# Kernel tuning notes

Measured on AMD Instinct MI355X. Metric: run time of the kernel, lower is better.

## Reference

```python
import jax, jax.numpy as jnp
import numpy as np

jax.config.update("jax_enable_x64", True)  # faithful int64 LIF state, as in the torch module

NUM_INPUTS = 700
NUM_HIDDEN = 4096
NUM_OUTPUT = 20
N_STEPS = 1000
ALPHA_SHIFT = 4   # synaptic-current decay shift
BETA_SHIFT = 3    # membrane decay shift
THRESHOLD = 1
BW1 = 64
BW2 = 64


def _sat(x, bw):
    # Quantize.saturate + to_int: clamp to signed bw-bit range, cast to int64.
    lo = -(2 ** (bw - 1))
    hi = 2 ** (bw - 1) - 1
    if jnp.issubdtype(x.dtype, jnp.floating):
        # values here are far below 2**63, so the float clip/cast is exact
        return jnp.clip(x, float(lo), float(hi)).astype(jnp.int64)
    return jnp.clip(x, lo, hi)


def _decay(v, shift):
    # LIF.exp_decay: v - (v >> shift) with arithmetic right shift on int64
    return v - (v >> shift)


def setup_inputs() -> dict:
    key = jax.random.key(0)
    k1, k2, k3, k4 = jax.random.split(key, 4)
    input_spikes = jax.random.randint(k1, (N_STEPS, NUM_INPUTS), 0, 2, dtype=jnp.int64)
    w1 = jax.random.randint(k2, (NUM_HIDDEN, NUM_INPUTS), -8, 8, dtype=jnp.int64)
    v1 = jax.random.randint(k3, (NUM_HIDDEN, NUM_HIDDEN), -8, 8, dtype=jnp.int64)
    w2 = jax.random.randint(k4, (NUM_OUTPUT, NUM_HIDDEN), -8, 8, dtype=jnp.int64)
    return {"input_spikes": input_spikes, "w1": w1, "v1": v1, "w2": w2}


def reference(input_spikes, w1, v1, w2):
    w1f = w1.astype(jnp.float32)
    v1f = v1.astype(jnp.float32)
    w2f = w2.astype(jnp.float32)
    # feed-forward input currents for all timesteps at once: [T, H]
    in_all = _sat(jnp.einsum("hi,ti->th", w1f, input_spikes.astype(jnp.float32)), BW1)

    H = w1.shape[0]
    O = w2.shape[0]
    z = lambda n: jnp.zeros((n,), dtype=jnp.int64)
    # state: hidden spikes, hidden mem, hidden syn, readout mem, readout syn
    init = (z(H), z(H), z(H), z(O), z(O))

    def step(state, in_cur):
        h_out, h_mem, h_syn, r_mem, r_syn = state
        # recurrent feedback current from PREVIOUS step's hidden spikes
        fb = _sat(jnp.einsum("hk,k->h", v1f, h_out.astype(jnp.float32)), BW1)
        syn_curr = _sat(in_cur + fb, BW1)
        # hidden LIF: reset (by previous spike) -> threshold -> decay/integrate
        h_mem = jnp.where(h_out == 1, 0, h_mem)
        new_out = (h_mem - THRESHOLD > 0).astype(jnp.int64)
        new_mem = _decay(h_mem, BETA_SHIFT) + h_syn
        new_syn = _decay(h_syn, ALPHA_SHIFT) + syn_curr
        # readout LIF (no reset); records updated membrane
        ro_cur = _sat(jnp.einsum("oh,h->o", w2f, new_out.astype(jnp.float32)), BW2)
        new_rmem = _decay(r_mem, BETA_SHIFT) + r_syn
        new_rsyn = _decay(r_syn, ALPHA_SHIFT) + ro_cur
        return (new_out, new_mem, new_syn, new_rmem, new_rsyn), new_rmem

    _, rec = jax.lax.scan(step, init, in_all)  # rec: [T, O]
    return rec.T  # torch.stack(ro_mem_rec, dim=1) -> [num_output, n_steps]
```

## Files before the change

kernel.cpp:

```cpp
#include <hip/hip_runtime.h>

#define T_STEPS 1000
#define N_IN    700
#define N_HID   4096
#define N_OUT   20
#define NBLK    64
#define HPB     64

typedef unsigned int u32x4 __attribute__((ext_vector_type(4)));

__device__ __forceinline__ u32x4 load_rec(const u32x4* p) {
    u32x4 r;
    asm volatile("global_load_dwordx4 %0, %1, off sc0 sc1\n\t"
                 "s_waitcnt vmcnt(0)"
                 : "=v"(r) : "v"(p) : "memory");
    return r;
}
__device__ __forceinline__ void store_rec(u32x4* p, u32x4 v) {
    asm volatile("global_store_dwordx4 %0, %1, off sc0 sc1"
                 :: "v"(p), "v"(v) : "memory");
}

__global__ __launch_bounds__(256) void k_transpose_i8(
    const int* __restrict__ in, signed char* __restrict__ out,
    int R, int C, int out_stride)
{
    __shared__ signed char tile[32][33];
    const int cx = blockIdx.x * 32;
    const int ry = blockIdx.y * 32;
    const int tx = threadIdx.x;
    const int ty = threadIdx.y;
#pragma unroll
    for (int r = 0; r < 4; ++r) {
        int row = ry + ty + r * 8;
        int col = cx + tx;
        if (row < R && col < C)
            tile[ty + r * 8][tx] = (signed char)in[(size_t)row * C + col];
    }
    __syncthreads();
#pragma unroll
    for (int r = 0; r < 4; ++r) {
        int c   = cx + ty + r * 8;
        int row = ry + tx;
        if (c < C && row < R)
            out[(size_t)c * out_stride + row] = tile[tx][ty + r * 8];
    }
}

__global__ __launch_bounds__(256) void k_prep_v1(
    const int* __restrict__ in, unsigned char* __restrict__ out)
{
    __shared__ unsigned char tile[32][33];
    const int kx = blockIdx.x * 32;
    const int hy = blockIdx.y * 32;
    const int tx = threadIdx.x;
    const int ty = threadIdx.y;
#pragma unroll
    for (int r = 0; r < 4; ++r) {
        int h = hy + ty + r * 8;
        tile[ty + r * 8][tx] = (unsigned char)(in[(size_t)h * N_HID + kx + tx] + 8);
    }
    __syncthreads();
    const size_t bofs = (size_t)(hy >> 6) * (N_HID * 64) + (hy & 32);
#pragma unroll
    for (int r = 0; r < 4; ++r) {
        int k = kx + ty + r * 8;
        out[bofs + ((size_t)k << 6) + tx] = tile[tx][ty + r * 8];
    }
}

__global__ __launch_bounds__(256) void k_inall(
    const signed char* __restrict__ w1t,
    const int* __restrict__ spk,
    short* __restrict__ in_all)
{
    __shared__ int s_spk[16][N_IN];
    const int t0 = blockIdx.y * 16;
    const int tcnt = min(16, T_STEPS - t0);
    const int tid = threadIdx.x;
    for (int b = 0; b < tcnt; ++b)
        for (int i = tid; i < N_IN; i += 256)
            s_spk[b][i] = spk[(size_t)(t0 + b) * N_IN + i];
    __syncthreads();
    const int h = blockIdx.x * 256 + tid;
    int acc[16];
#pragma unroll
    for (int b = 0; b < 16; ++b) acc[b] = 0;
    for (int i = 0; i < N_IN; ++i) {
        int w = (int)w1t[(size_t)i * N_HID + h];
#pragma unroll
        for (int b = 0; b < 16; ++b) acc[b] += w * s_spk[b][i];
    }
    for (int b = 0; b < tcnt; ++b)
        in_all[(size_t)(t0 + b) * N_HID + h] = (short)acc[b];
}

__global__ __launch_bounds__(256) void k_main(
    const short* __restrict__ in_all,
    const unsigned char* __restrict__ v1b,
    u32x4* __restrict__ pub)
{
    const int tid  = threadIdx.x;
    const int wave = tid >> 6;
    const int lane = tid & 63;
    const int hb   = blockIdx.x * HPB;

    __shared__ unsigned short s_list[N_HID];
    __shared__ unsigned int s_part[4][4][8];
    __shared__ int s_n;

    int mt = 0, syn = 0, cur_out = 0;
    unsigned long long omask = 0;

    const unsigned char* gbase = v1b + ((size_t)blockIdx.x << 18) + ((lane & 3) << 4);
    const int wg = (wave << 4) | (lane >> 2);

    for (int t = 0; t < T_STEPS; ++t) {
        int in_cur = 0;
        if (wave == 0) {
            if (lane == 0) {
                u32x4 v = { (unsigned)omask, (unsigned)(omask >> 32), 1u, 0u };
                store_rec(pub + (size_t)t * NBLK + blockIdx.x, v);
            }
            in_cur = (int)in_all[(size_t)t * N_HID + hb + lane];
            unsigned long long kmask = 0;
            if (t > 0) {
                const u32x4* rec = pub + (size_t)(t - 1) * NBLK + lane;
                u32x4 r = load_rec(rec);
                while (r.z == 0u) { __builtin_amdgcn_s_sleep(1); r = load_rec(rec); }
                kmask = ((unsigned long long)r.y << 32) | (unsigned long long)r.x;
            }
            int cnt = __popcll(kmask);
            int inc = cnt;
#pragma unroll
            for (int d = 1; d < 64; d <<= 1) {
                int v = __shfl_up(inc, d);
                if (lane >= d) inc += v;
            }
            int p = inc - cnt;
            unsigned long long m = kmask;
            while (m) {
                s_list[p++] = (unsigned short)((lane << 6) | __builtin_ctzll(m));
                m &= m - 1;
            }
            if (lane == 63) s_n = inc;
        }
        __syncthreads();
        const int n = s_n;

        unsigned int a0=0,a1=0,a2=0,a3=0,a4=0,a5=0,a6=0,a7=0;
#pragma unroll 8
        for (int j = wg; j < n; j += 64) {
            int k = s_list[j];
            u32x4 v = *(const u32x4*)(gbase + ((size_t)k << 6));
            const unsigned int M = 0x00FF00FFu;
            a0 += v.x & M;  a1 += (v.x >> 8) & M;
            a2 += v.y & M;  a3 += (v.y >> 8) & M;
            a4 += v.z & M;  a5 += (v.z >> 8) & M;
            a6 += v.w & M;  a7 += (v.w >> 8) & M;
        }
#pragma unroll
        for (int s = 4; s <= 32; s <<= 1) {
            a0 += __shfl_xor(a0, s); a1 += __shfl_xor(a1, s);
            a2 += __shfl_xor(a2, s); a3 += __shfl_xor(a3, s);
            a4 += __shfl_xor(a4, s); a5 += __shfl_xor(a5, s);
            a6 += __shfl_xor(a6, s); a7 += __shfl_xor(a7, s);
        }
        if (lane < 4) {
            unsigned int* sp = s_part[wave][lane];
            sp[0]=a0; sp[1]=a1; sp[2]=a2; sp[3]=a3;
            sp[4]=a4; sp[5]=a5; sp[6]=a6; sp[7]=a7;
        }
        __syncthreads();

        if (wave == 0) {
            const int li = lane >> 4, b = lane & 15;
            const int c = ((b >> 2) << 1) | (b & 1);
            const int half = (b >> 1) & 1;
            unsigned int s = s_part[0][li][c] + s_part[1][li][c]
                           + s_part[2][li][c] + s_part[3][li][c];
            int fb = (int)((s >> (half << 4)) & 0xFFFFu) - 8 * n;

            int new_mem = (mt - (mt >> 3)) + syn;
            syn = (syn - (syn >> 4)) + in_cur + fb;
            mt = cur_out ? 0 : new_mem;
            cur_out = (mt - 1 > 0) ? 1 : 0;
            omask = __ballot(cur_out);
        }
    }
}

__global__ __launch_bounds__(256) void k_rocur(
    const int* __restrict__ w2,
    const u32x4* __restrict__ pub,
    int* __restrict__ ro)
{
    const int t = blockIdx.x;
    const int tid = threadIdx.x;
    __shared__ unsigned short s_list[N_HID];
    __shared__ int s_red[32][8];
    __shared__ int s_n;
    if (tid < 64) {
        u32x4 rec = pub[(size_t)t * NBLK + tid];
        unsigned long long m = (unsigned long long)rec.x |
                               ((unsigned long long)rec.y << 32);
        int cnt = __popcll(m);
        int inc = cnt;
#pragma unroll
        for (int d = 1; d < 64; d <<= 1) {
            int v = __shfl_up(inc, d);
            if (tid >= d) inc += v;
        }
        int p = inc - cnt;
        while (m) {
            s_list[p++] = (unsigned short)((tid << 6) | __builtin_ctzll(m));
            m &= m - 1;
        }
        if (tid == 63) s_n = inc;
    }
    __syncthreads();
    const int n = s_n;
    const int o = tid >> 3;
    const int r = tid & 7;
    if (o < N_OUT) {
        int acc = 0;
        for (int j = r; j < n; j += 8) acc += w2[(size_t)o * N_HID + s_list[j]];
        s_red[o][r] = acc;
    }
    __syncthreads();
    if (tid < N_OUT) {
        int acc = 0;
#pragma unroll
        for (int q = 0; q < 8; ++q) acc += s_red[tid][q];
        ro[(size_t)t * N_OUT + tid] = acc;
    }
}

#define CH 250
__global__ __launch_bounds__(256) void k_scan(const int* __restrict__ ro,
                                              int* __restrict__ out)
{
    __shared__ int s_ro[CH * N_OUT];
    const int tid = threadIdx.x;
    int rm = 0, rs = 0;
    for (int c = 0; c < T_STEPS / CH; ++c) {
        __syncthreads();
        for (int i = tid; i < CH * N_OUT; i += 256)
            s_ro[i] = ro[c * CH * N_OUT + i];
        __syncthreads();
        if (tid < N_OUT) {
            for (int j = 0; j < CH; ++j) {
                rm = (rm - (rm >> 3)) + rs;
                rs = (rs - (rs >> 4)) + s_ro[j * N_OUT + tid];
                out[tid * T_STEPS + c * CH + j] = rm;
            }
        }
    }
}

extern "C" void kernel_launch(void* const* d_in, const int* in_sizes, int n_in,
                              void* d_out, int out_size, void* d_ws, size_t ws_size,
                              hipStream_t stream)
{
    const int* spk = (const int*)d_in[0];
    const int* w1  = (const int*)d_in[1];
    const int* v1  = (const int*)d_in[2];
    const int* w2  = (const int*)d_in[3];
    int* out = (int*)d_out;

    char* ws = (char*)d_ws;
    constexpr size_t SZ_PUB    = (size_t)T_STEPS * NBLK * 16;
    constexpr size_t OFF_PUB   = 0;
    constexpr size_t OFF_INALL = OFF_PUB + SZ_PUB;
    constexpr size_t OFF_V1B   = OFF_INALL + 8192000;
    constexpr size_t OFF_W1T   = OFF_V1B + 16777216;
    constexpr size_t OFF_RO    = OFF_W1T + 2867200;

    u32x4*          pub    = (u32x4*)(ws + OFF_PUB);
    short*          in_all = (short*)(ws + OFF_INALL);
    unsigned char*  v1b    = (unsigned char*)(ws + OFF_V1B);
    signed char*    w1t    = (signed char*)(ws + OFF_W1T);
    int*            ro     = (int*)(ws + OFF_RO);

    hipMemsetAsync(pub, 0, SZ_PUB, stream);

    dim3 tb(32, 8);
    k_prep_v1<<<dim3(128, 128), tb, 0, stream>>>(v1, v1b);
    k_transpose_i8<<<dim3(22, 128), tb, 0, stream>>>(w1, w1t, N_HID, N_IN, N_HID);
    k_inall<<<dim3(16, 63), 256, 0, stream>>>(w1t, spk, in_all);

    k_main<<<dim3(NBLK), dim3(256), 0, stream>>>(in_all, v1b, pub);

    k_rocur<<<dim3(T_STEPS), 256, 0, stream>>>(w2, pub, ro);
    k_scan<<<1, 256, 0, stream>>>(ro, out);
}
```

Measured before the change: 1.754 ms.

## Restructure recurrent step to publish spikes early and prefetch records via LDS

The LIF membrane/spike update is reordered so the next step's spike mask is computed and published before the feedback reduction, shortening the critical path between blocks. Spike records are prefetched asynchronously into LDS with global_load_lds, falling back to polling only when not yet ready. The list build is spread across all four waves, each compacting its own 16-bit fragment instead of wave 0 doing it alone. in_all is re-laid out per block for contiguous reads, and the readout scan's output is staged in shared memory for coalesced stores. This adds double-buffered shared state and relies on an early prefetch often seeing stale data.

New measurement: 1.594 ms. 9.1% less time.

```diff
diff --git a/kernel.cpp b/kernel.cpp
--- a/kernel.cpp
+++ b/kernel.cpp
@@ -9,7 +9,7 @@
 
 typedef unsigned int u32x4 __attribute__((ext_vector_type(4)));
 
-__device__ __forceinline__ u32x4 load_rec(const u32x4* p) {
+__device__ __forceinline__ u32x4 load_rec_sync(const u32x4* p) {
     u32x4 r;
     asm volatile("global_load_dwordx4 %0, %1, off sc0 sc1\n\t"
                  "s_waitcnt vmcnt(0)"
@@ -72,7 +72,7 @@
 __global__ __launch_bounds__(256) void k_inall(
     const signed char* __restrict__ w1t,
     const int* __restrict__ spk,
-    short* __restrict__ in_all)
+    short* __restrict__ in_all2)
 {
     __shared__ int s_spk[16][N_IN];
     const int t0 = blockIdx.y * 16;
@@ -91,67 +91,93 @@
 #pragma unroll
         for (int b = 0; b < 16; ++b) acc[b] += w * s_spk[b][i];
     }
+    const size_t base = (size_t)(h >> 6) * (T_STEPS * 64) + (h & 63);
     for (int b = 0; b < tcnt; ++b)
-        in_all[(size_t)(t0 + b) * N_HID + h] = (short)acc[b];
+        in_all2[base + (size_t)(t0 + b) * 64] = (short)acc[b];
 }
 
 __global__ __launch_bounds__(256) void k_main(
-    const short* __restrict__ in_all,
+    const short* __restrict__ in_all2,
     const unsigned char* __restrict__ v1b,
     u32x4* __restrict__ pub)
 {
     const int tid  = threadIdx.x;
     const int wave = tid >> 6;
     const int lane = tid & 63;
-    const int hb   = blockIdx.x * HPB;
-
-    __shared__ unsigned short s_list[N_HID];
-    __shared__ unsigned int s_part[4][4][8];
-    __shared__ int s_n;
-
-    int mt = 0, syn = 0, cur_out = 0;
-    unsigned long long omask = 0;
-
-    const unsigned char* gbase = v1b + ((size_t)blockIdx.x << 18) + ((lane & 3) << 4);
-    const int wg = (wave << 4) | (lane >> 2);
+    const int bid  = blockIdx.x;
+
+    __shared__ unsigned short s_list[4][1024];
+    __shared__ u32x4 s_rec[2][NBLK];
+    __shared__ unsigned int s_part[2][4][4][8];
+    __shared__ int s_nw[2][4];
+
+    int mm = 0, synv = 0, out_t = 0;
+
+    const unsigned char* gbase = v1b + ((size_t)bid << 18) + ((lane & 3) << 4);
+    const int slot    = lane >> 2;
+    const int mb      = (wave << 4) | slot;
+    const int frag_sh = (lane & 3) << 4;
+    const int kbase   = (mb << 6) + frag_sh;
+    const short* in_base = in_all2 + (size_t)bid * (T_STEPS * 64) + lane;
+
+    if (tid == 0) { u32x4 v = {0u, 0u, 1u, 0u}; store_rec(pub + bid, v); }
+    __syncthreads();
 
     for (int t = 0; t < T_STEPS; ++t) {
+        const int cur = t & 1;
         int in_cur = 0;
         if (wave == 0) {
+            int mem_t = (mm - (mm >> 3)) + synv;
+            int mnext = out_t ? 0 : mem_t;
+            int out_n = (mnext - 1 > 0) ? 1 : 0;
+            unsigned long long om = __ballot(out_n);
             if (lane == 0) {
-                u32x4 v = { (unsigned)omask, (unsigned)(omask >> 32), 1u, 0u };
-                store_rec(pub + (size_t)t * NBLK + blockIdx.x, v);
+                u32x4 v = {(unsigned)om, (unsigned)(om >> 32), 1u, 0u};
+                store_rec(pub + (size_t)(t + 1) * NBLK + bid, v);
             }
-            in_cur = (int)in_all[(size_t)t * N_HID + hb + lane];
-            unsigned long long kmask = 0;
-            if (t > 0) {
-                const u32x4* rec = pub + (size_t)(t - 1) * NBLK + lane;
-                u32x4 r = load_rec(rec);
-                while (r.z == 0u) { __builtin_amdgcn_s_sleep(1); r = load_rec(rec); }
-                kmask = ((unsigned long long)r.y << 32) | (unsigned long long)r.x;
+            in_cur = (int)in_base[t * 64];
+            mm = mnext; out_t = out_n;
+        }
+
+        unsigned int frag = 0;
+        if (t > 0) {
+            u32x4 rec = s_rec[cur][mb];
+            if (rec.z == 0u) {
+                const u32x4* rp = pub + (size_t)(t - 1) * NBLK + mb;
+                do { __builtin_amdgcn_s_sleep(1); rec = load_rec_sync(rp); }
+                while (rec.z == 0u);
             }
-            int cnt = __popcll(kmask);
-            int inc = cnt;
-#pragma unroll
-            for (int d = 1; d < 64; d <<= 1) {
-                int v = __shfl_up(inc, d);
-                if (lane >= d) inc += v;
-            }
-            int p = inc - cnt;
-            unsigned long long m = kmask;
-            while (m) {
-                s_list[p++] = (unsigned short)((lane << 6) | __builtin_ctzll(m));
-                m &= m - 1;
-            }
-            if (lane == 63) s_n = inc;
-        }
-        __syncthreads();
-        const int n = s_n;
+            unsigned long long km = ((unsigned long long)rec.y << 32) |
+                                     (unsigned long long)rec.x;
+            frag = (unsigned int)((km >> frag_sh) & 0xFFFFull);
+        }
+        int cnt = __popc(frag);
+        int inc = cnt;
+#pragma unroll
+        for (int d = 1; d < 64; d <<= 1) {
+            int v = __shfl_up(inc, d);
+            if (lane >= d) inc += v;
+        }
+        int p = inc - cnt;
+        unsigned int m = frag;
+        while (m) {
+            s_list[wave][p++] = (unsigned short)(kbase + __builtin_ctz(m));
+            m &= m - 1;
+        }
+        const int n_w = __shfl(inc, 63);
+        if (lane == 0) s_nw[cur][wave] = n_w;
+
+        if (wave == 0)
+            __builtin_amdgcn_global_load_lds(
+                (const void*)(pub + (size_t)t * NBLK + lane),
+                (void*)&s_rec[cur ^ 1][0], 16, 0,  17);
+
+        asm volatile("s_waitcnt lgkmcnt(0)" ::: "memory");
 
         unsigned int a0=0,a1=0,a2=0,a3=0,a4=0,a5=0,a6=0,a7=0;
 #pragma unroll 8
-        for (int j = wg; j < n; j += 64) {
-            int k = s_list[j];
+        for (int j = slot; j < n_w; j += 16) {
+            int k = s_list[wave][j];
             u32x4 v = *(const u32x4*)(gbase + ((size_t)k << 6));
             const unsigned int M = 0x00FF00FFu;
             a0 += v.x & M;  a1 += (v.x >> 8) & M;
@@ -167,25 +193,21 @@
             a6 += __shfl_xor(a6, s); a7 += __shfl_xor(a7, s);
         }
         if (lane < 4) {
-            unsigned int* sp = s_part[wave][lane];
+            unsigned int* sp = s_part[cur][wave][lane];
             sp[0]=a0; sp[1]=a1; sp[2]=a2; sp[3]=a3;
             sp[4]=a4; sp[5]=a5; sp[6]=a6; sp[7]=a7;
         }
         __syncthreads();
 
         if (wave == 0) {
+            const int n = s_nw[cur][0] + s_nw[cur][1] + s_nw[cur][2] + s_nw[cur][3];
             const int li = lane >> 4, b = lane & 15;
             const int c = ((b >> 2) << 1) | (b & 1);
             const int half = (b >> 1) & 1;
-            unsigned int s = s_part[0][li][c] + s_part[1][li][c]
-                           + s_part[2][li][c] + s_part[3][li][c];
+            unsigned int s = s_part[cur][0][li][c] + s_part[cur][1][li][c]
+                           + s_part[cur][2][li][c] + s_part[cur][3][li][c];
             int fb = (int)((s >> (half << 4)) & 0xFFFFu) - 8 * n;
-
-            int new_mem = (mt - (mt >> 3)) + syn;
-            syn = (syn - (syn >> 4)) + in_cur + fb;
-            mt = cur_out ? 0 : new_mem;
-            cur_out = (mt - 1 > 0) ? 1 : 0;
-            omask = __ballot(cur_out);
+            synv = (synv - (synv >> 4)) + in_cur + fb;
         }
     }
 }
@@ -241,10 +263,10 @@
                                               int* __restrict__ out)
 {
     __shared__ int s_ro[CH * N_OUT];
+    __shared__ int s_out[CH * N_OUT];
     const int tid = threadIdx.x;
     int rm = 0, rs = 0;
     for (int c = 0; c < T_STEPS / CH; ++c) {
-        __syncthreads();
         for (int i = tid; i < CH * N_OUT; i += 256)
             s_ro[i] = ro[c * CH * N_OUT + i];
         __syncthreads();
@@ -252,9 +274,15 @@
             for (int j = 0; j < CH; ++j) {
                 rm = (rm - (rm >> 3)) + rs;
                 rs = (rs - (rs >> 4)) + s_ro[j * N_OUT + tid];
-                out[tid * T_STEPS + c * CH + j] = rm;
+                s_out[j * N_OUT + tid] = rm;
             }
         }
+        __syncthreads();
+        for (int i = tid; i < CH * N_OUT; i += 256) {
+            int o = i / CH, j = i - o * CH;
+            out[o * T_STEPS + c * CH + j] = s_out[j * N_OUT + o];
+        }
+        __syncthreads();
     }
 }
 
@@ -269,7 +297,7 @@
     int* out = (int*)d_out;
 
     char* ws = (char*)d_ws;
-    constexpr size_t SZ_PUB    = (size_t)T_STEPS * NBLK * 16;
+    constexpr size_t SZ_PUB    = (size_t)(T_STEPS + 1) * NBLK * 16;
     constexpr size_t OFF_PUB   = 0;
     constexpr size_t OFF_INALL = OFF_PUB + SZ_PUB;
     constexpr size_t OFF_V1B   = OFF_INALL + 8192000;
```
